# Performance work log

Hardware: AMD Instinct MI355X
Metric: run time of the kernel (lower is better)

Reference implementation:

```python
import jax, jax.numpy as jnp
import numpy as np

B, N, C = 8, 1024, 1024
H = 16
D = C // H  # head_dim = 64
SCALE = D ** -0.5


def setup_inputs() -> dict:
    key = jax.random.key(0)
    k1, k2, k3 = jax.random.split(key, 3)
    x = jax.random.normal(k1, (B, N, C), dtype=jnp.float32)
    w_qkv = jax.random.normal(k2, (3 * C, C), dtype=jnp.float32) * (C ** -0.5)
    w_proj = jax.random.normal(k3, (C, C), dtype=jnp.float32) * (C ** -0.5)
    b_proj = jnp.zeros((C,), dtype=jnp.float32)
    return {"x": x, "w_qkv": w_qkv, "w_proj": w_proj, "b_proj": b_proj}


def reference(x, w_qkv, w_proj, b_proj):
    Bx, Nx, Cx = x.shape
    # qkv: [B,N,3C] -> [3,B,H,N,D]
    qkv = jnp.einsum('bnc,oc->bno', x, w_qkv)
    qkv = qkv.reshape(Bx, Nx, 3, H, D).transpose(2, 0, 3, 1, 4)
    q, k, v = qkv[0], qkv[1], qkv[2]
    attn = jnp.einsum('bhnd,bhmd->bhnm', q, k) * SCALE  # [B,H,N,N]
    attn = jax.nn.softmax(attn, axis=-1)
    out = jnp.einsum('bhnm,bhmd->bhnd', attn, v)  # [B,H,N,D]
    out = out.transpose(0, 2, 1, 3).reshape(Bx, Nx, Cx)
    return jnp.einsum('bnc,oc->bno', out, w_proj) + b_proj
```

## Files before the change

kernel.cpp:

```cpp
#include <hip/hip_runtime.h>

typedef _Float16 half8 __attribute__((ext_vector_type(8)));
typedef _Float16 half4v __attribute__((ext_vector_type(4)));
typedef _Float16 half2v __attribute__((ext_vector_type(2)));
typedef float floatx4 __attribute__((ext_vector_type(4)));

#define AS3 __attribute__((address_space(3)))
#define AS1 __attribute__((address_space(1)))

__global__ __launch_bounds__(256) void cvt_f32_f16(const float* __restrict__ in,
                                                   _Float16* __restrict__ out, int n4) {
    int i = blockIdx.x * 256 + threadIdx.x;
    if (i >= n4) return;
    float4 v = ((const float4*)in)[i];
    half4v h = {(_Float16)v.x, (_Float16)v.y, (_Float16)v.z, (_Float16)v.w};
    ((half4v*)out)[i] = h;
}

__global__ __launch_bounds__(256) void gemm_tn(
    const _Float16* __restrict__ A, const _Float16* __restrict__ B,
    _Float16* __restrict__ Ch, int ldc, _Float16* __restrict__ Ch2, int ldc2, int split,
    float* __restrict__ Cf, const float* __restrict__ bias,
    int M, int Nn, int K)
{
    __shared__ _Float16 sA[2][128 * 32];
    __shared__ _Float16 sB[2][128 * 32];
    const int tid  = threadIdx.x;
    const int lane = tid & 63, wave = tid >> 6;
    const int quad = lane >> 4, l16 = lane & 15;
    const int wr = wave >> 1, wc = wave & 1;
    const long m0 = (long)blockIdx.x * 128, n0 = (long)blockIdx.y * 128;

    const int srow = tid >> 2;
    const int scol = (((tid & 3) ^ ((srow >> 1) & 3)) * 8);
    const _Float16* gA0 = A + (m0 + srow) * (long)K + scol;
    const _Float16* gA1 = A + (m0 + srow + 64) * (long)K + scol;
    const _Float16* gB0 = B + (n0 + srow) * (long)K + scol;
    const _Float16* gB1 = B + (n0 + srow + 64) * (long)K + scol;
    AS3 _Float16* sA3 = (AS3 _Float16*)&sA[0][0];
    AS3 _Float16* sB3 = (AS3 _Float16*)&sB[0][0];
    const int lo0 = tid * 8, lo1 = (tid + 256) * 8;

    const int swz = (l16 >> 1) & 3;
    const int aoff = ((quad ^ swz) * 8);

    floatx4 acc[4][4] = {};

    const int nk = K >> 5;
    __builtin_amdgcn_global_load_lds((const AS1 void*)gA0, (AS3 void*)(sA3 + lo0), 16, 0, 0);
    __builtin_amdgcn_global_load_lds((const AS1 void*)gA1, (AS3 void*)(sA3 + lo1), 16, 0, 0);
    __builtin_amdgcn_global_load_lds((const AS1 void*)gB0, (AS3 void*)(sB3 + lo0), 16, 0, 0);
    __builtin_amdgcn_global_load_lds((const AS1 void*)gB1, (AS3 void*)(sB3 + lo1), 16, 0, 0);

    for (int kk = 0; kk < nk; kk++) {
        const int cur = kk & 1;
        __syncthreads();
        if (kk + 1 < nk) {
            const int nb = (cur ^ 1) * 4096;
            const long k0 = (long)(kk + 1) << 5;
            __builtin_amdgcn_global_load_lds((const AS1 void*)(gA0 + k0), (AS3 void*)(sA3 + nb + lo0), 16, 0, 0);
            __builtin_amdgcn_global_load_lds((const AS1 void*)(gA1 + k0), (AS3 void*)(sA3 + nb + lo1), 16, 0, 0);
            __builtin_amdgcn_global_load_lds((const AS1 void*)(gB0 + k0), (AS3 void*)(sB3 + nb + lo0), 16, 0, 0);
            __builtin_amdgcn_global_load_lds((const AS1 void*)(gB1 + k0), (AS3 void*)(sB3 + nb + lo1), 16, 0, 0);
        }
        const _Float16* cA = &sA[cur][0];
        const _Float16* cB = &sB[cur][0];

        half8 af[4], bf[4];
#pragma unroll
        for (int t = 0; t < 4; t++)
            af[t] = *(const half8*)&cA[(wr * 64 + t * 16 + l16) * 32 + aoff];
#pragma unroll
        for (int t = 0; t < 4; t++)
            bf[t] = *(const half8*)&cB[(wc * 64 + t * 16 + l16) * 32 + aoff];
#pragma unroll
        for (int tm = 0; tm < 4; tm++)
#pragma unroll
            for (int tn = 0; tn < 4; tn++)
                acc[tm][tn] = __builtin_amdgcn_mfma_f32_16x16x32_f16(af[tm], bf[tn], acc[tm][tn], 0, 0, 0);
    }

    const bool useC2 = (Cf == nullptr) && (n0 >= split);
#pragma unroll
    for (int tm = 0; tm < 4; tm++) {
        long row = m0 + wr * 64 + tm * 16 + quad * 4;
#pragma unroll
        for (int tn = 0; tn < 4; tn++) {
            long col = n0 + wc * 64 + tn * 16 + l16;
            float bv = bias ? bias[col] : 0.f;
#pragma unroll
            for (int r = 0; r < 4; r++) {
                float v = acc[tm][tn][r];
                if (Cf)        Cf[(row + r) * (long)Nn + col] = v + bv;
                else if (useC2) Ch2[(row + r) * (long)ldc2 + (col - split)] = (_Float16)v;
                else           Ch[(row + r) * (long)ldc + col] = (_Float16)v;
            }
        }
    }
}

__global__ __launch_bounds__(256) void transpose_v(const _Float16* __restrict__ vh,
                                                   _Float16* __restrict__ vt) {
    const int bh = blockIdx.x;
    const int b = bh >> 4, h = bh & 15;
    const int n0 = blockIdx.y * 64;
    const int d = threadIdx.x & 63;
    const int ng = threadIdx.x >> 6;
#pragma unroll
    for (int i = 0; i < 2; i++) {
        int nb = (ng + 4 * i) * 8;
        half8 vv;
#pragma unroll
        for (int j = 0; j < 8; j++)
            vv[j] = vh[(long)(b * 1024 + n0 + nb + j) * 1024 + h * 64 + d];
        *(half8*)&vt[((long)(bh * 64 + d)) * 1024 + n0 + nb] = vv;
    }
}

#define CSC 0.125f
__global__ __launch_bounds__(256, 4) void flash_attn(const _Float16* __restrict__ qk,
                                                     const _Float16* __restrict__ vt,
                                                     _Float16* __restrict__ out)
{
    const int bh = blockIdx.x, b = bh >> 4, h = bh & 15;
    const int n0 = blockIdx.y * 128;
    const int tid = threadIdx.x, lane = tid & 63, wave = tid >> 6;
    const int quad = lane >> 4, l16 = lane & 15;

    __shared__ _Float16 sK[64 * 72];
    __shared__ _Float16 sVT[64 * 72];
    __shared__ _Float16 sPT[4][32 * 72];

    half8 qf[2][2];
    const _Float16* qbase = qk + (long)(b * 1024 + n0 + wave * 32) * 2048 + h * 64;
#pragma unroll
    for (int t = 0; t < 2; t++)
#pragma unroll
        for (int s = 0; s < 2; s++)
            qf[t][s] = *(const half8*)(qbase + (long)(t * 16 + l16) * 2048 + s * 32 + quad * 8);

    const int srow = tid >> 3, scol8 = (tid & 7) * 8;
    const _Float16* kgb = qk + 1024 + h * 64 + scol8 + (long)(b * 1024 + srow) * 2048;
    const _Float16* vgb = vt + (long)(bh * 64 + srow) * 1024 + scol8;

    float m_[2] = {-1e30f, -1e30f}, l_[2] = {0.f, 0.f};
    floatx4 o[2][4] = {};

    for (int kt = 0; kt < 16; kt++) {
        const int kr0 = kt * 64;
        __syncthreads();
#pragma unroll
        for (int i = 0; i < 2; i++) {
            int r = srow + i * 32;
            *(half8*)&sK[r * 72 + scol8]  = *(const half8*)(kgb + (long)(kr0 + i * 32) * 2048);
            *(half8*)&sVT[r * 72 + scol8] = *(const half8*)(vgb + (long)(i * 32) * 1024 + kr0);
        }
        __syncthreads();

        floatx4 sacc[2][4] = {};
#pragma unroll
        for (int c = 0; c < 4; c++)
#pragma unroll
            for (int s = 0; s < 2; s++) {
                half8 kf = *(const half8*)&sK[(c * 16 + l16) * 72 + s * 32 + quad * 8];
                sacc[0][c] = __builtin_amdgcn_mfma_f32_16x16x32_f16(kf, qf[0][s], sacc[0][c], 0, 0, 0);
                sacc[1][c] = __builtin_amdgcn_mfma_f32_16x16x32_f16(kf, qf[1][s], sacc[1][c], 0, 0, 0);
            }

#pragma unroll
        for (int t = 0; t < 2; t++) {
            float mx = -1e30f;
#pragma unroll
            for (int c = 0; c < 4; c++)
#pragma unroll
                for (int r = 0; r < 4; r++) {
                    float v = sacc[t][c][r] * CSC;
                    sacc[t][c][r] = v;
                    mx = fmaxf(mx, v);
                }
            mx = fmaxf(mx, __shfl_xor(mx, 16));
            mx = fmaxf(mx, __shfl_xor(mx, 32));
            float mn = fmaxf(m_[t], mx);
            float al = __expf(m_[t] - mn);
            m_[t] = mn;
            float rs = 0.f;
#pragma unroll
            for (int c = 0; c < 4; c++)
#pragma unroll
                for (int r = 0; r < 4; r++) {
                    float p = __expf(sacc[t][c][r] - mn);
                    sacc[t][c][r] = p;
                    rs += p;
                }
            rs += __shfl_xor(rs, 16);
            rs += __shfl_xor(rs, 32);
            l_[t] = l_[t] * al + rs;
#pragma unroll
            for (int dt = 0; dt < 4; dt++) o[t][dt] *= al;
#pragma unroll
            for (int c = 0; c < 4; c++) {
                half2v p01 = {(_Float16)sacc[t][c][0], (_Float16)sacc[t][c][1]};
                half2v p23 = {(_Float16)sacc[t][c][2], (_Float16)sacc[t][c][3]};
                *(half2v*)&sPT[wave][(t * 16 + l16) * 72 + c * 16 + quad * 4]     = p01;
                *(half2v*)&sPT[wave][(t * 16 + l16) * 72 + c * 16 + quad * 4 + 2] = p23;
            }
        }

#pragma unroll
        for (int kk = 0; kk < 2; kk++) {
            half8 pf0 = *(const half8*)&sPT[wave][(l16) * 72 + kk * 32 + quad * 8];
            half8 pf1 = *(const half8*)&sPT[wave][(16 + l16) * 72 + kk * 32 + quad * 8];
#pragma unroll
            for (int dt = 0; dt < 4; dt++) {
                half8 vf = *(const half8*)&sVT[(dt * 16 + l16) * 72 + kk * 32 + quad * 8];
                o[0][dt] = __builtin_amdgcn_mfma_f32_16x16x32_f16(vf, pf0, o[0][dt], 0, 0, 0);
                o[1][dt] = __builtin_amdgcn_mfma_f32_16x16x32_f16(vf, pf1, o[1][dt], 0, 0, 0);
            }
        }
    }

#pragma unroll
    for (int t = 0; t < 2; t++) {
        float inv = 1.f / l_[t];
#pragma unroll
        for (int dt = 0; dt < 4; dt++) {
            floatx4 v = o[t][dt];
            half2v a = {(_Float16)(v[0] * inv), (_Float16)(v[1] * inv)};
            half2v c = {(_Float16)(v[2] * inv), (_Float16)(v[3] * inv)};
            *(half2v*)&sPT[wave][(t * 16 + l16) * 72 + dt * 16 + quad * 4]     = a;
            *(half2v*)&sPT[wave][(t * 16 + l16) * 72 + dt * 16 + quad * 4 + 2] = c;
        }
    }
    __syncthreads();
#pragma unroll
    for (int i = 0; i < 4; i++) {
        int ql = i * 8 + (lane >> 3);
        int c8 = (lane & 7) * 8;
        half8 vv = *(const half8*)&sPT[wave][ql * 72 + c8];
        *(half8*)(out + (long)(b * 1024 + n0 + wave * 32 + ql) * 1024 + h * 64 + c8) = vv;
    }
}

extern "C" void kernel_launch(void* const* d_in, const int* in_sizes, int n_in,
                              void* d_out, int out_size, void* d_ws, size_t ws_size,
                              hipStream_t stream) {
    const float* x      = (const float*)d_in[0];
    const float* w_qkv  = (const float*)d_in[1];
    const float* w_proj = (const float*)d_in[2];
    const float* b_proj = (const float*)d_in[3];

    char* ws = (char*)d_ws;
    _Float16* qkh    = (_Float16*)ws;
    _Float16* vh     = (_Float16*)(ws + 33554432);
    _Float16* xh     = (_Float16*)(ws + 50331648);
    _Float16* wqkvh  = (_Float16*)(ws + 67108864);
    _Float16* wprojh = (_Float16*)(ws + 73400320);
    _Float16* vT     = xh;
    _Float16* attnh  = vh;

    cvt_f32_f16<<<8192, 256, 0, stream>>>(x, xh, 8388608 / 4);
    cvt_f32_f16<<<3072, 256, 0, stream>>>(w_qkv, wqkvh, 3145728 / 4);
    cvt_f32_f16<<<1024, 256, 0, stream>>>(w_proj, wprojh, 1048576 / 4);

    gemm_tn<<<dim3(64, 24), 256, 0, stream>>>(xh, wqkvh, qkh, 2048, vh, 1024, 2048,
                                              nullptr, nullptr, 8192, 3072, 1024);
    transpose_v<<<dim3(128, 16), 256, 0, stream>>>(vh, vT);
    flash_attn<<<dim3(128, 8), 256, 0, stream>>>(qkh, vT, attnh);
    gemm_tn<<<dim3(64, 8), 256, 0, stream>>>(attnh, wprojh, nullptr, 0, nullptr, 0, 1 << 30,
                                             (float*)d_out, b_proj, 8192, 1024, 1024);
}
```

Baseline: 265.4 us.

## Replace direct global-to-LDS loads with register-staged prefetch in GEMM

```diff
diff --git a/kernel.cpp b/kernel.cpp
--- a/kernel.cpp
+++ b/kernel.cpp
@@ -17,7 +17,7 @@
     ((half4v*)out)[i] = h;
 }
 
-__global__ __launch_bounds__(256) void gemm_tn(
+__global__ __launch_bounds__(256, 3) void gemm_tn(
     const _Float16* __restrict__ A, const _Float16* __restrict__ B,
     _Float16* __restrict__ Ch, int ldc, _Float16* __restrict__ Ch2, int ldc2, int split,
     float* __restrict__ Cf, const float* __restrict__ bias,
@@ -32,40 +32,37 @@
     const long m0 = (long)blockIdx.x * 128, n0 = (long)blockIdx.y * 128;
 
     const int srow = tid >> 2;
-    const int scol = (((tid & 3) ^ ((srow >> 1) & 3)) * 8);
-    const _Float16* gA0 = A + (m0 + srow) * (long)K + scol;
-    const _Float16* gA1 = A + (m0 + srow + 64) * (long)K + scol;
-    const _Float16* gB0 = B + (n0 + srow) * (long)K + scol;
-    const _Float16* gB1 = B + (n0 + srow + 64) * (long)K + scol;
-    AS3 _Float16* sA3 = (AS3 _Float16*)&sA[0][0];
-    AS3 _Float16* sB3 = (AS3 _Float16*)&sB[0][0];
-    const int lo0 = tid * 8, lo1 = (tid + 256) * 8;
+    const int sslot = ((tid & 3) ^ ((srow >> 1) & 3)) * 8;
+    const int dlo = srow * 32 + sslot;
+    const int dhi = (srow + 64) * 32 + sslot;
+    const _Float16* gA0 = A + (m0 + srow) * (long)K + (tid & 3) * 8;
+    const _Float16* gA1 = A + (m0 + srow + 64) * (long)K + (tid & 3) * 8;
+    const _Float16* gB0 = B + (n0 + srow) * (long)K + (tid & 3) * 8;
+    const _Float16* gB1 = B + (n0 + srow + 64) * (long)K + (tid & 3) * 8;
 
     const int swz = (l16 >> 1) & 3;
     const int aoff = ((quad ^ swz) * 8);
 
     floatx4 acc[4][4] = {};
-
     const int nk = K >> 5;
-    __builtin_amdgcn_global_load_lds((const AS1 void*)gA0, (AS3 void*)(sA3 + lo0), 16, 0, 0);
-    __builtin_amdgcn_global_load_lds((const AS1 void*)gA1, (AS3 void*)(sA3 + lo1), 16, 0, 0);
-    __builtin_amdgcn_global_load_lds((const AS1 void*)gB0, (AS3 void*)(sB3 + lo0), 16, 0, 0);
-    __builtin_amdgcn_global_load_lds((const AS1 void*)gB1, (AS3 void*)(sB3 + lo1), 16, 0, 0);
+
+    half8 rA0 = *(const half8*)gA0, rA1 = *(const half8*)gA1;
+    half8 rB0 = *(const half8*)gB0, rB1 = *(const half8*)gB1;
+    *(half8*)&sA[0][dlo] = rA0; *(half8*)&sA[0][dhi] = rA1;
+    *(half8*)&sB[0][dlo] = rB0; *(half8*)&sB[0][dhi] = rB1;
 
     for (int kk = 0; kk < nk; kk++) {
         const int cur = kk & 1;
         __syncthreads();
-        if (kk + 1 < nk) {
-            const int nb = (cur ^ 1) * 4096;
+        const bool more = (kk + 1 < nk);
+        if (more) {
             const long k0 = (long)(kk + 1) << 5;
-            __builtin_amdgcn_global_load_lds((const AS1 void*)(gA0 + k0), (AS3 void*)(sA3 + nb + lo0), 16, 0, 0);
-            __builtin_amdgcn_global_load_lds((const AS1 void*)(gA1 + k0), (AS3 void*)(sA3 + nb + lo1), 16, 0, 0);
-            __builtin_amdgcn_global_load_lds((const AS1 void*)(gB0 + k0), (AS3 void*)(sB3 + nb + lo0), 16, 0, 0);
-            __builtin_amdgcn_global_load_lds((const AS1 void*)(gB1 + k0), (AS3 void*)(sB3 + nb + lo1), 16, 0, 0);
-        }
+            rA0 = *(const half8*)(gA0 + k0); rA1 = *(const half8*)(gA1 + k0);
+            rB0 = *(const half8*)(gB0 + k0); rB1 = *(const half8*)(gB1 + k0);
+        }
+
         const _Float16* cA = &sA[cur][0];
         const _Float16* cB = &sB[cur][0];
-
         half8 af[4], bf[4];
 #pragma unroll
         for (int t = 0; t < 4; t++)
@@ -78,6 +75,13 @@
 #pragma unroll
             for (int tn = 0; tn < 4; tn++)
                 acc[tm][tn] = __builtin_amdgcn_mfma_f32_16x16x32_f16(af[tm], bf[tn], acc[tm][tn], 0, 0, 0);
+
+        if (more) {
+            _Float16* nA = &sA[cur ^ 1][0];
+            _Float16* nB = &sB[cur ^ 1][0];
+            *(half8*)&nA[dlo] = rA0; *(half8*)&nA[dhi] = rA1;
+            *(half8*)&nB[dlo] = rB0; *(half8*)&nB[dhi] = rB1;
+        }
     }
 
     const bool useC2 = (Cf == nullptr) && (n0 >= split);
```

After: 265.9 us. Within noise of the previous version (+0.2%).
